# Kernel tuning notes

Measured on AMD Instinct MI355X. Metric: run time of the kernel, lower is better.

The kernel has to match this reference:

```python
import jax, jax.numpy as jnp
import numpy as np

H = 1024           # hidden_size
E = 8              # num_experts
I = 4096 // E      # expert_intermediate_size = 512
V = 32000          # vocab_size
T = 4096           # num_tokens


def setup_inputs() -> dict:
    key = jax.random.key(0)
    ks = jax.random.split(key, 6)
    x = jax.random.normal(ks[0], (T, H), dtype=jnp.float32)
    token_ids = jax.random.randint(ks[1], (T,), 0, V, dtype=jnp.int64)
    mu = jax.random.normal(ks[2], (T, H), dtype=jnp.float32)
    # learned parameters (kaiming-like scale)
    gate_up_proj = jax.random.normal(ks[3], (E, H, 2 * I), dtype=jnp.float32) * (1.0 / np.sqrt(H))
    down_proj = jax.random.normal(ks[4], (E, I, H), dtype=jnp.float32) * (1.0 / np.sqrt(I))
    mu_w = jax.random.normal(ks[5], (E, H), dtype=jnp.float32) * 0.02  # mu_router.weight [E, H]
    return {"x": x, "token_ids": token_ids, "mu": mu,
            "gate_up_proj": gate_up_proj, "down_proj": down_proj, "mu_w": mu_w}


def reference(x, token_ids, mu, gate_up_proj, down_proj, mu_w):
    # deterministic base routing: expert = token_id % num_experts
    tid = jnp.clip(token_ids, 0, V - 1)
    base_expert = tid % E                                   # [T]
    # mu router biases the routing decision
    mu_logits = mu @ mu_w.T                                 # [T, E]
    combined = jax.nn.one_hot(base_expert, E, dtype=jnp.float32) * 10.0 + mu_logits
    expert_ids = jnp.argmax(combined, axis=-1)              # [T]

    out = jnp.zeros_like(x)
    # fixed small loop over experts; rows not routed to e are discarded by the mask,
    # so computing the dense GEMM over all tokens gives identical selected rows.
    for e in range(E):
        mask = (expert_ids == e)                            # [T]
        gu = x @ gate_up_proj[e]                            # [T, 2I]
        gate, up = gu[:, :I], gu[:, I:]
        inter = jax.nn.silu(gate) * up                      # [T, I]
        y = inter @ down_proj[e]                            # [T, H]
        out = jnp.where(mask[:, None], y, out)
    return out
```

## Files before the change

### kernel.cpp

```cpp
#include <hip/hip_runtime.h>
#include <cmath>

constexpr int T_DIM = 4096;
constexpr int H_DIM = 1024;
constexpr int E_DIM = 8;
constexpr int I_DIM = 512;
constexpr int V_DIM = 32000;

typedef _Float16 half_t;
typedef __attribute__((ext_vector_type(8))) _Float16 halfx8;
typedef __attribute__((ext_vector_type(4))) _Float16 halfx4;
typedef __attribute__((ext_vector_type(4))) float floatx4;

#define GLOAD16(g, l)                                                        \
    __builtin_amdgcn_global_load_lds(                                        \
        (const __attribute__((address_space(1))) void*)(g),                  \
        (__attribute__((address_space(3))) void*)(l), 16, 0, 0)

constexpr int  CNT_STRIDE  = 16;
constexpr size_t OFF_COUNTS = 0;
constexpr size_t OFF_EID    = 1024;
constexpr size_t OFF_TOKL   = OFF_EID + (size_t)T_DIM * 4;
constexpr size_t OFF_XB     = OFF_TOKL + (size_t)E_DIM * T_DIM * 4;
constexpr size_t OFF_GUPT   = OFF_XB + (size_t)T_DIM * H_DIM * 2;
constexpr size_t OFF_DOWNT  = OFF_GUPT + (size_t)E_DIM * 2 * I_DIM * H_DIM * 2;
constexpr size_t OFF_INTER  = OFF_DOWNT + (size_t)E_DIM * H_DIM * I_DIM * 2;

__global__ __launch_bounds__(256) void prep_kernel(
    const float* __restrict__ x, const float* __restrict__ gup,
    const float* __restrict__ mu, const int* __restrict__ token_ids,
    const float* __restrict__ mu_w, half_t* __restrict__ xb,
    half_t* __restrict__ gupT, int* __restrict__ expert_id)
{
    const int z = blockIdx.z, bx = blockIdx.x, by = blockIdx.y;
    const int tid = threadIdx.x;

    if (z >= 1) {
        const int t = ((z - 1) * 256 + by) * 8 + bx;

        const float4 xv = *(const float4*)&x[(size_t)t * H_DIM + tid * 4];

        const float4 m = *(const float4*)&mu[(size_t)t * H_DIM + tid * 4];
        float acc[E_DIM];
#pragma unroll
        for (int e = 0; e < E_DIM; ++e) {
            const float4 w = *(const float4*)&mu_w[e * H_DIM + tid * 4];
            acc[e] = m.x * w.x + m.y * w.y + m.z * w.z + m.w * w.w;
        }

        halfx4 xh = { (half_t)xv.x, (half_t)xv.y, (half_t)xv.z, (half_t)xv.w };
        *(halfx4*)&xb[(size_t)t * H_DIM + tid * 4] = xh;

#pragma unroll
        for (int e = 0; e < E_DIM; ++e) {
#pragma unroll
            for (int off = 32; off > 0; off >>= 1)
                acc[e] += __shfl_down(acc[e], off, 64);
        }
        __shared__ float part[4][E_DIM];
        const int lane = tid & 63, w = tid >> 6;
        if (lane == 0) {
#pragma unroll
            for (int e = 0; e < E_DIM; ++e) part[w][e] = acc[e];
        }
        __syncthreads();
        if (tid == 0) {
            int tk = token_ids[t];
            tk = min(max(tk, 0), V_DIM - 1);
            const int be = tk & (E_DIM - 1);
            float best = -1e30f; int bi = 0;
#pragma unroll
            for (int e = 0; e < E_DIM; ++e) {
                const float c = part[0][e] + part[1][e] + part[2][e] + part[3][e]
                              + (e == be ? 10.f : 0.f);
                if (c > best) { best = c; bi = e; }
            }
            expert_id[t] = bi;
        }
        return;
    }

    __shared__ float tile[64][65];
    const float* se = gup + (size_t)bx * H_DIM * (2 * I_DIM);
    half_t* de = gupT + (size_t)bx * (2 * I_DIM) * H_DIM;
    constexpr int N = 1024, K = H_DIM;
    const int n0 = (by & 15) * 64, k0 = (by >> 4) * 64;
    const int c4 = (tid & 15) * 4, r0 = tid >> 4;
#pragma unroll
    for (int p = 0; p < 4; ++p) {
        const int r = r0 + p * 16;
        const float4 v = *(const float4*)&se[(size_t)(k0 + r) * N + n0 + c4];
        tile[r][c4 + 0] = v.x; tile[r][c4 + 1] = v.y;
        tile[r][c4 + 2] = v.z; tile[r][c4 + 3] = v.w;
    }
    __syncthreads();
    const int kc8 = (tid & 7) * 8, nb = tid >> 3;
#pragma unroll
    for (int p = 0; p < 2; ++p) {
        const int n = nb + p * 32;
        halfx8 h = { (half_t)tile[kc8 + 0][n], (half_t)tile[kc8 + 1][n],
                     (half_t)tile[kc8 + 2][n], (half_t)tile[kc8 + 3][n],
                     (half_t)tile[kc8 + 4][n], (half_t)tile[kc8 + 5][n],
                     (half_t)tile[kc8 + 6][n], (half_t)tile[kc8 + 7][n] };
        *(halfx8*)&de[(size_t)(n0 + n) * K + k0 + kc8] = h;
    }
}

__global__ __launch_bounds__(1024) void scatter_kernel(
    const int* __restrict__ expert_id, int* __restrict__ counts,
    int* __restrict__ tok_list)
{
    const int e = blockIdx.x;
    const int tid = threadIdx.x;
    const int lane = tid & 63, wv = tid >> 6;
    __shared__ int wcnt[16];
    int base = 0;
#pragma unroll
    for (int r = 0; r < 4; ++r) {
        const int t = r * 1024 + tid;
        const bool m = (expert_id[t] == e);
        const unsigned long long mask = __ballot(m);
        const int wrank = (int)__popcll(mask & ((1ull << lane) - 1ull));
        if (lane == 0) wcnt[wv] = (int)__popcll(mask);
        __syncthreads();
        int pre = 0, tot = 0;
#pragma unroll
        for (int i = 0; i < 16; ++i) {
            const int c = wcnt[i];
            pre += (i < wv) ? c : 0;
            tot += c;
        }
        if (m) tok_list[e * T_DIM + base + pre + wrank] = t;
        base += tot;
        __syncthreads();
    }
    if (tid == 0) counts[e * CNT_STRIDE] = base;
}

__global__ __launch_bounds__(256) void gemm1_mfma_kernel(
    const half_t* __restrict__ xb, const half_t* __restrict__ gupT,
    const float* __restrict__ down, half_t* __restrict__ downT,
    const int* __restrict__ counts, const int* __restrict__ tok_list,
    half_t* __restrict__ inter)
{
    __shared__ __align__(16) char smraw[49152 + 64 * 4];
    const int tid = threadIdx.x;
    const int e = blockIdx.x;

    if (blockIdx.z >= 64) {
        float (*tile)[65] = (float (*)[65])smraw;
        const float* se = down + (size_t)e * I_DIM * H_DIM;
        half_t* de = downT + (size_t)e * H_DIM * I_DIM;
        const int n0 = (blockIdx.z - 64) * 64, k0 = blockIdx.y * 64;
        const int c4 = (tid & 15) * 4, r0 = tid >> 4;
#pragma unroll
        for (int p = 0; p < 4; ++p) {
            const int r = r0 + p * 16;
            const float4 v = *(const float4*)&se[(size_t)(k0 + r) * H_DIM + n0 + c4];
            tile[r][c4 + 0] = v.x; tile[r][c4 + 1] = v.y;
            tile[r][c4 + 2] = v.z; tile[r][c4 + 3] = v.w;
        }
        __syncthreads();
        const int kc8 = (tid & 7) * 8, nb = tid >> 3;
#pragma unroll
        for (int p = 0; p < 2; ++p) {
            const int n = nb + p * 32;
            halfx8 h = { (half_t)tile[kc8 + 0][n], (half_t)tile[kc8 + 1][n],
                         (half_t)tile[kc8 + 2][n], (half_t)tile[kc8 + 3][n],
                         (half_t)tile[kc8 + 4][n], (half_t)tile[kc8 + 5][n],
                         (half_t)tile[kc8 + 6][n], (half_t)tile[kc8 + 7][n] };
            *(halfx8*)&de[(size_t)(n0 + n) * I_DIM + k0 + kc8] = h;
        }
        return;
    }

    const int count = counts[e * CNT_STRIDE];
    const int m0 = blockIdx.z * 64;
    if (m0 >= count) return;
    const int n0 = blockIdx.y * 64;

    half_t* const As0 = (half_t*)smraw;
    half_t* const As1 = (half_t*)(smraw + 8192);
    half_t* const Bs0 = (half_t*)(smraw + 16384);
    half_t* const Bs1 = (half_t*)(smraw + 32768);
    int* const toks = (int*)(smraw + 49152);

    if (tid < 64) {
        const int m = m0 + tid;
        toks[tid] = (m < count) ? tok_list[e * T_DIM + m] : -1;
    }
    __syncthreads();

    const half_t* We = gupT + (size_t)e * (2 * I_DIM) * H_DIM;

    const int lane = tid & 63;
    const int w = tid >> 6;
    const int lr = lane >> 3, lc = lane & 7;

    const half_t* aptr[2]; const half_t* bptr[4];
    half_t *a0l[2], *a1l[2], *b0l[4], *b1l[4];
#pragma unroll
    for (int j = 0; j < 2; ++j) {
        const int r = w * 16 + j * 8 + lr;
        const int cg = lc ^ (r & 7);
        const int tk = toks[r];
        aptr[j] = xb + (size_t)(tk < 0 ? 0 : tk) * H_DIM + cg * 8;
        const int off = (w * 16 + j * 8) * 64;
        a0l[j] = As0 + off; a1l[j] = As1 + off;
    }
#pragma unroll
    for (int j = 0; j < 4; ++j) {
        const int n = w * 32 + j * 8 + lr;
        const int col = (n < 64) ? (n0 + n) : (I_DIM + n0 + (n - 64));
        const int cg = lc ^ (n & 7);
        bptr[j] = We + (size_t)col * H_DIM + cg * 8;
        const int off = (w * 32 + j * 8) * 64;
        b0l[j] = Bs0 + off; b1l[j] = Bs1 + off;
    }

    const floatx4 fzero = {0.f, 0.f, 0.f, 0.f};
    floatx4 accg[2][2], accu[2][2];
#pragma unroll
    for (int i = 0; i < 2; ++i)
#pragma unroll
        for (int j = 0; j < 2; ++j) { accg[i][j] = fzero; accu[i][j] = fzero; }

    const int wr = w >> 1, wc = w & 1;
    const int fm = lane & 15, q = lane >> 4;
    const int fm7 = fm & 7;

    auto mfma_phase = [&](const half_t* A_, const half_t* B_) {
#pragma unroll
        for (int ks = 0; ks < 2; ++ks) {
            const int swz = ((ks * 4 + q) ^ fm7) * 8;
            const halfx8 a0 = *(const halfx8*)&A_[(32 * wr + fm) * 64 + swz];
            const halfx8 a1 = *(const halfx8*)&A_[(32 * wr + 16 + fm) * 64 + swz];
#pragma unroll
            for (int ct = 0; ct < 2; ++ct) {
                const int ng = wc * 32 + ct * 16 + fm;
                const halfx8 bg = *(const halfx8*)&B_[ng * 64 + swz];
                const halfx8 bu = *(const halfx8*)&B_[(64 + ng) * 64 + swz];
                accg[0][ct] = __builtin_amdgcn_mfma_f32_16x16x32_f16(a0, bg, accg[0][ct], 0, 0, 0);
                accg[1][ct] = __builtin_amdgcn_mfma_f32_16x16x32_f16(a1, bg, accg[1][ct], 0, 0, 0);
                accu[0][ct] = __builtin_amdgcn_mfma_f32_16x16x32_f16(a0, bu, accu[0][ct], 0, 0, 0);
                accu[1][ct] = __builtin_amdgcn_mfma_f32_16x16x32_f16(a1, bu, accu[1][ct], 0, 0, 0);
            }
        }
    };

#pragma unroll
    for (int j = 0; j < 2; ++j) GLOAD16(aptr[j], a0l[j]);
#pragma unroll
    for (int j = 0; j < 4; ++j) GLOAD16(bptr[j], b0l[j]);
#pragma unroll
    for (int j = 0; j < 2; ++j) GLOAD16(aptr[j] + 64, a1l[j]);
#pragma unroll
    for (int j = 0; j < 4; ++j) GLOAD16(bptr[j] + 64, b1l[j]);

    constexpr int NSTEP1 = H_DIM / 64;
#pragma unroll
    for (int it = 0; it < NSTEP1; ++it) {
        if (it < NSTEP1 - 1) asm volatile("s_waitcnt vmcnt(6)" ::: "memory");
        else                 asm volatile("s_waitcnt vmcnt(0)" ::: "memory");
        __builtin_amdgcn_s_barrier();
        __builtin_amdgcn_sched_barrier(0);
        __builtin_amdgcn_s_setprio(1);
        if ((it & 1) == 0) mfma_phase(As0, Bs0);
        else               mfma_phase(As1, Bs1);
        __builtin_amdgcn_s_setprio(0);
        asm volatile("s_waitcnt lgkmcnt(0)" ::: "memory");
        __builtin_amdgcn_sched_barrier(0);
        __builtin_amdgcn_s_barrier();
        __builtin_amdgcn_sched_barrier(0);
        const int k2 = (it + 2) * 64;
        if (k2 < H_DIM) {
            if ((it & 1) == 0) {
#pragma unroll
                for (int j = 0; j < 2; ++j) GLOAD16(aptr[j] + k2, a0l[j]);
#pragma unroll
                for (int j = 0; j < 4; ++j) GLOAD16(bptr[j] + k2, b0l[j]);
            } else {
#pragma unroll
                for (int j = 0; j < 2; ++j) GLOAD16(aptr[j] + k2, a1l[j]);
#pragma unroll
                for (int j = 0; j < 4; ++j) GLOAD16(bptr[j] + k2, b1l[j]);
            }
        }
    }

#pragma unroll
    for (int rt = 0; rt < 2; ++rt)
#pragma unroll
        for (int r = 0; r < 4; ++r) {
            const int row = 32 * wr + 16 * rt + q * 4 + r;
            const int tk = toks[row];
            if (tk < 0) continue;
#pragma unroll
            for (int ct = 0; ct < 2; ++ct) {
                const float g = accg[rt][ct][r];
                const float u = accu[rt][ct][r];
                const float s = g / (1.f + __expf(-g)) * u;
                inter[(size_t)tk * I_DIM + n0 + wc * 32 + ct * 16 + fm] = (half_t)s;
            }
        }
}

__global__ __launch_bounds__(256) void gemm2_mfma_kernel(
    const half_t* __restrict__ inter, const half_t* __restrict__ downT,
    const int* __restrict__ counts, const int* __restrict__ tok_list,
    float* __restrict__ out)
{
    const int e = blockIdx.x;
    const int count = counts[e * CNT_STRIDE];
    const int m0 = blockIdx.z * 64;
    if (m0 >= count) return;
    const int n0 = blockIdx.y * 128;

    __shared__ __align__(16) char smraw[49152 + 64 * 4];
    half_t* const As0 = (half_t*)smraw;
    half_t* const As1 = (half_t*)(smraw + 8192);
    half_t* const Bs0 = (half_t*)(smraw + 16384);
    half_t* const Bs1 = (half_t*)(smraw + 32768);
    int* const toks = (int*)(smraw + 49152);

    const int tid = threadIdx.x;
    if (tid < 64) {
        const int m = m0 + tid;
        toks[tid] = (m < count) ? tok_list[e * T_DIM + m] : -1;
    }
    __syncthreads();

    const half_t* De = downT + (size_t)e * H_DIM * I_DIM;

    const int lane = tid & 63;
    const int w = tid >> 6;
    const int lr = lane >> 3, lc = lane & 7;

    const half_t* aptr[2]; const half_t* bptr[4];
    half_t *a0l[2], *a1l[2], *b0l[4], *b1l[4];
#pragma unroll
    for (int j = 0; j < 2; ++j) {
        const int r = w * 16 + j * 8 + lr;
        const int cg = lc ^ (r & 7);
        const int tk = toks[r];
        aptr[j] = inter + (size_t)(tk < 0 ? 0 : tk) * I_DIM + cg * 8;
        const int off = (w * 16 + j * 8) * 64;
        a0l[j] = As0 + off; a1l[j] = As1 + off;
    }
#pragma unroll
    for (int j = 0; j < 4; ++j) {
        const int n = w * 32 + j * 8 + lr;
        const int cg = lc ^ (n & 7);
        bptr[j] = De + (size_t)(n0 + n) * I_DIM + cg * 8;
        const int off = (w * 32 + j * 8) * 64;
        b0l[j] = Bs0 + off; b1l[j] = Bs1 + off;
    }

    const floatx4 fzero = {0.f, 0.f, 0.f, 0.f};
    floatx4 acc[2][4];
#pragma unroll
    for (int i = 0; i < 2; ++i)
#pragma unroll
        for (int j = 0; j < 4; ++j) acc[i][j] = fzero;

    const int wr = w >> 1, wc = w & 1;
    const int fm = lane & 15, q = lane >> 4;
    const int fm7 = fm & 7;

    auto mfma_phase = [&](const half_t* A_, const half_t* B_) {
#pragma unroll
        for (int ks = 0; ks < 2; ++ks) {
            const int swz = ((ks * 4 + q) ^ fm7) * 8;
            const halfx8 a0 = *(const halfx8*)&A_[(32 * wr + fm) * 64 + swz];
            const halfx8 a1 = *(const halfx8*)&A_[(32 * wr + 16 + fm) * 64 + swz];
#pragma unroll
            for (int ct = 0; ct < 4; ++ct) {
                const halfx8 b = *(const halfx8*)&B_[(wc * 64 + ct * 16 + fm) * 64 + swz];
                acc[0][ct] = __builtin_amdgcn_mfma_f32_16x16x32_f16(a0, b, acc[0][ct], 0, 0, 0);
                acc[1][ct] = __builtin_amdgcn_mfma_f32_16x16x32_f16(a1, b, acc[1][ct], 0, 0, 0);
            }
        }
    };

#pragma unroll
    for (int j = 0; j < 2; ++j) GLOAD16(aptr[j], a0l[j]);
#pragma unroll
    for (int j = 0; j < 4; ++j) GLOAD16(bptr[j], b0l[j]);
#pragma unroll
    for (int j = 0; j < 2; ++j) GLOAD16(aptr[j] + 64, a1l[j]);
#pragma unroll
    for (int j = 0; j < 4; ++j) GLOAD16(bptr[j] + 64, b1l[j]);

    constexpr int NSTEP2 = I_DIM / 64;
#pragma unroll
    for (int it = 0; it < NSTEP2; ++it) {
        if (it < NSTEP2 - 1) asm volatile("s_waitcnt vmcnt(6)" ::: "memory");
        else                 asm volatile("s_waitcnt vmcnt(0)" ::: "memory");
        __builtin_amdgcn_s_barrier();
        __builtin_amdgcn_sched_barrier(0);
        __builtin_amdgcn_s_setprio(1);
        if ((it & 1) == 0) mfma_phase(As0, Bs0);
        else               mfma_phase(As1, Bs1);
        __builtin_amdgcn_s_setprio(0);
        asm volatile("s_waitcnt lgkmcnt(0)" ::: "memory");
        __builtin_amdgcn_sched_barrier(0);
        __builtin_amdgcn_s_barrier();
        __builtin_amdgcn_sched_barrier(0);
        const int k2 = (it + 2) * 64;
        if (k2 < I_DIM) {
            if ((it & 1) == 0) {
#pragma unroll
                for (int j = 0; j < 2; ++j) GLOAD16(aptr[j] + k2, a0l[j]);
#pragma unroll
                for (int j = 0; j < 4; ++j) GLOAD16(bptr[j] + k2, b0l[j]);
            } else {
#pragma unroll
                for (int j = 0; j < 2; ++j) GLOAD16(aptr[j] + k2, a1l[j]);
#pragma unroll
                for (int j = 0; j < 4; ++j) GLOAD16(bptr[j] + k2, b1l[j]);
            }
        }
    }

#pragma unroll
    for (int rt = 0; rt < 2; ++rt)
#pragma unroll
        for (int r = 0; r < 4; ++r) {
            const int row = 32 * wr + 16 * rt + q * 4 + r;
            const int tk = toks[row];
            if (tk < 0) continue;
#pragma unroll
            for (int ct = 0; ct < 4; ++ct)
                out[(size_t)tk * H_DIM + n0 + wc * 64 + ct * 16 + fm] = acc[rt][ct][r];
        }
}

extern "C" void kernel_launch(void* const* d_in, const int* in_sizes, int n_in,
                              void* d_out, int out_size, void* d_ws, size_t ws_size,
                              hipStream_t stream)
{
    const float* x         = (const float*)d_in[0];
    const int*   token_ids = (const int*)  d_in[1];
    const float* mu        = (const float*)d_in[2];
    const float* gup       = (const float*)d_in[3];
    const float* down      = (const float*)d_in[4];
    const float* mu_w      = (const float*)d_in[5];
    float* out = (float*)d_out;

    char* ws = (char*)d_ws;
    int*    counts    = (int*)(ws + OFF_COUNTS);
    int*    expert_id = (int*)(ws + OFF_EID);
    int*    tok_list  = (int*)(ws + OFF_TOKL);
    half_t* xb        = (half_t*)(ws + OFF_XB);
    half_t* gupT      = (half_t*)(ws + OFF_GUPT);
    half_t* downT     = (half_t*)(ws + OFF_DOWNT);
    half_t* inter     = (half_t*)(ws + OFF_INTER);

    prep_kernel<<<dim3(8, 256, 3), 256, 0, stream>>>(
        x, gup, mu, token_ids, mu_w, xb, gupT, expert_id);
    scatter_kernel<<<E_DIM, 1024, 0, stream>>>(expert_id, counts, tok_list);
    gemm1_mfma_kernel<<<dim3(E_DIM, 8, 80), 256, 0, stream>>>(
        xb, gupT, down, downT, counts, tok_list, inter);
    gemm2_mfma_kernel<<<dim3(E_DIM, 8, T_DIM / 64), 256, 0, stream>>>(
        inter, downT, counts, tok_list, out);
}
```

Measured before the change: 157.0 us.

## Fuse scatter into prep kernel via atomic completion counters

Removes the separate scatter kernel launch. Its work now runs in eight blocks of the prep grid that spin on per-group atomic done counters until every routing block has written its expert ids. Routing is also reworked so each wavefront handles one token with xor-shuffle reductions instead of a block-wide shared-memory reduction. The in-kernel spin-wait depends on the producer blocks being scheduled alongside the waiting ones, which risks deadlock or stalls. It also adds a memset launch to reset the counters.

Measured after the change: 295.1 us. 1.88x slower.

```diff
diff --git a/kernel.cpp b/kernel.cpp
--- a/kernel.cpp
+++ b/kernel.cpp
@@ -25,58 +25,101 @@
 constexpr size_t OFF_GUPT   = OFF_XB + (size_t)T_DIM * H_DIM * 2;
 constexpr size_t OFF_DOWNT  = OFF_GUPT + (size_t)E_DIM * 2 * I_DIM * H_DIM * 2;
 constexpr size_t OFF_INTER  = OFF_DOWNT + (size_t)E_DIM * H_DIM * I_DIM * 2;
+constexpr size_t OFF_DONE   = OFF_INTER + (size_t)T_DIM * I_DIM * 2;
 
 __global__ __launch_bounds__(256) void prep_kernel(
     const float* __restrict__ x, const float* __restrict__ gup,
     const float* __restrict__ mu, const int* __restrict__ token_ids,
     const float* __restrict__ mu_w, half_t* __restrict__ xb,
-    half_t* __restrict__ gupT, int* __restrict__ expert_id)
+    half_t* __restrict__ gupT, int* __restrict__ expert_id,
+    int* __restrict__ counts, int* __restrict__ tok_list,
+    int* __restrict__ done)
 {
     const int z = blockIdx.z, bx = blockIdx.x, by = blockIdx.y;
     const int tid = threadIdx.x;
 
-    if (z >= 1) {
-        const int t = ((z - 1) * 256 + by) * 8 + bx;
-
-        const float4 xv = *(const float4*)&x[(size_t)t * H_DIM + tid * 4];
-
-        const float4 m = *(const float4*)&mu[(size_t)t * H_DIM + tid * 4];
+    if (z == 1) {
+        if (by >= 128) return;
+        const int rb = bx + 8 * by;
+        const int wv = tid >> 6, l = tid & 63;
+        const int t = rb * 4 + wv;
+        const size_t tb = (size_t)t * H_DIM;
+
         float acc[E_DIM];
 #pragma unroll
+        for (int e = 0; e < E_DIM; ++e) acc[e] = 0.f;
+#pragma unroll
+        for (int j = 0; j < 4; ++j) {
+            const int off = j * 256 + l * 4;
+            const float4 m4 = *(const float4*)&mu[tb + off];
+            const float4 x4 = *(const float4*)&x[tb + off];
+            halfx4 xh = { (half_t)x4.x, (half_t)x4.y, (half_t)x4.z, (half_t)x4.w };
+            *(halfx4*)&xb[tb + off] = xh;
+#pragma unroll
+            for (int e = 0; e < E_DIM; ++e) {
+                const float4 w = *(const float4*)&mu_w[e * H_DIM + off];
+                acc[e] += m4.x * w.x + m4.y * w.y + m4.z * w.z + m4.w * w.w;
+            }
+        }
+#pragma unroll
         for (int e = 0; e < E_DIM; ++e) {
-            const float4 w = *(const float4*)&mu_w[e * H_DIM + tid * 4];
-            acc[e] = m.x * w.x + m.y * w.y + m.z * w.z + m.w * w.w;
-        }
-
-        halfx4 xh = { (half_t)xv.x, (half_t)xv.y, (half_t)xv.z, (half_t)xv.w };
-        *(halfx4*)&xb[(size_t)t * H_DIM + tid * 4] = xh;
-
+#pragma unroll
+            for (int off = 1; off < 64; off <<= 1)
+                acc[e] += __shfl_xor(acc[e], off, 64);
+        }
+        int tk = token_ids[t];
+        tk = min(max(tk, 0), V_DIM - 1);
+        const int be = tk & (E_DIM - 1);
+        float best = -1e30f; int bi = 0;
 #pragma unroll
         for (int e = 0; e < E_DIM; ++e) {
-#pragma unroll
-            for (int off = 32; off > 0; off >>= 1)
-                acc[e] += __shfl_down(acc[e], off, 64);
-        }
-        __shared__ float part[4][E_DIM];
-        const int lane = tid & 63, w = tid >> 6;
-        if (lane == 0) {
-#pragma unroll
-            for (int e = 0; e < E_DIM; ++e) part[w][e] = acc[e];
+            const float c = acc[e] + (e == be ? 10.f : 0.f);
+            if (c > best) { best = c; bi = e; }
+        }
+        if (l == 0) {
+            expert_id[t] = bi;
+            __threadfence();
         }
         __syncthreads();
-        if (tid == 0) {
-            int tk = token_ids[t];
-            tk = min(max(tk, 0), V_DIM - 1);
-            const int be = tk & (E_DIM - 1);
-            float best = -1e30f; int bi = 0;
-#pragma unroll
-            for (int e = 0; e < E_DIM; ++e) {
-                const float c = part[0][e] + part[1][e] + part[2][e] + part[3][e]
-                              + (e == be ? 10.f : 0.f);
-                if (c > best) { best = c; bi = e; }
-            }
-            expert_id[t] = bi;
-        }
+        if (tid == 0)
+            __hip_atomic_fetch_add(&done[(rb & 63) * 16], 1,
+                                   __ATOMIC_RELEASE, __HIP_MEMORY_SCOPE_AGENT);
+        return;
+    }
+
+    if (z == 2) {
+        if (by != 0) return;
+        const int e = bx;
+        const int lane = tid & 63, wv = tid >> 6;
+        if (tid < 64) {
+            while (__hip_atomic_load(&done[tid * 16], __ATOMIC_ACQUIRE,
+                                     __HIP_MEMORY_SCOPE_AGENT) < 16)
+                __builtin_amdgcn_s_sleep(2);
+        }
+        __syncthreads();
+
+        __shared__ int wcnt[4];
+        int base = 0;
+#pragma unroll 1
+        for (int r = 0; r < 16; ++r) {
+            const int t = r * 256 + tid;
+            const bool m = (expert_id[t] == e);
+            const unsigned long long mask = __ballot(m);
+            const int wrank = (int)__popcll(mask & ((1ull << lane) - 1ull));
+            if (lane == 0) wcnt[wv] = (int)__popcll(mask);
+            __syncthreads();
+            int pre = 0, tot = 0;
+#pragma unroll
+            for (int i = 0; i < 4; ++i) {
+                const int c = wcnt[i];
+                pre += (i < wv) ? c : 0;
+                tot += c;
+            }
+            if (m) tok_list[e * T_DIM + base + pre + wrank] = t;
+            base += tot;
+            __syncthreads();
+        }
+        if (tid == 0) counts[e * CNT_STRIDE] = base;
         return;
     }
 
@@ -104,37 +147,6 @@
                      (half_t)tile[kc8 + 6][n], (half_t)tile[kc8 + 7][n] };
         *(halfx8*)&de[(size_t)(n0 + n) * K + k0 + kc8] = h;
     }
-}
-
-__global__ __launch_bounds__(1024) void scatter_kernel(
-    const int* __restrict__ expert_id, int* __restrict__ counts,
-    int* __restrict__ tok_list)
-{
-    const int e = blockIdx.x;
-    const int tid = threadIdx.x;
-    const int lane = tid & 63, wv = tid >> 6;
-    __shared__ int wcnt[16];
-    int base = 0;
-#pragma unroll
-    for (int r = 0; r < 4; ++r) {
-        const int t = r * 1024 + tid;
-        const bool m = (expert_id[t] == e);
-        const unsigned long long mask = __ballot(m);
-        const int wrank = (int)__popcll(mask & ((1ull << lane) - 1ull));
-        if (lane == 0) wcnt[wv] = (int)__popcll(mask);
-        __syncthreads();
-        int pre = 0, tot = 0;
-#pragma unroll
-        for (int i = 0; i < 16; ++i) {
-            const int c = wcnt[i];
-            pre += (i < wv) ? c : 0;
-            tot += c;
-        }
-        if (m) tok_list[e * T_DIM + base + pre + wrank] = t;
-        base += tot;
-        __syncthreads();
-    }
-    if (tid == 0) counts[e * CNT_STRIDE] = base;
 }
 
 __global__ __launch_bounds__(256) void gemm1_mfma_kernel(
@@ -455,10 +467,13 @@
     half_t* gupT      = (half_t*)(ws + OFF_GUPT);
     half_t* downT     = (half_t*)(ws + OFF_DOWNT);
     half_t* inter     = (half_t*)(ws + OFF_INTER);
+    int*    done      = (int*)(ws + OFF_DONE);
+
+    hipMemsetAsync(done, 0, 64 * CNT_STRIDE * sizeof(int), stream);
 
     prep_kernel<<<dim3(8, 256, 3), 256, 0, stream>>>(
-        x, gup, mu, token_ids, mu_w, xb, gupT, expert_id);
-    scatter_kernel<<<E_DIM, 1024, 0, stream>>>(expert_id, counts, tok_list);
+        x, gup, mu, token_ids, mu_w, xb, gupT, expert_id,
+        counts, tok_list, done);
     gemm1_mfma_kernel<<<dim3(E_DIM, 8, 80), 256, 0, stream>>>(
         xb, gupT, down, downT, counts, tok_list, inter);
     gemm2_mfma_kernel<<<dim3(E_DIM, 8, T_DIM / 64), 256, 0, stream>>>(
```
